# Optimization experiments

Hardware: AMD Instinct MI355X
Metric: run time of the kernel (lower is better)

## Reference

```python
import jax, jax.numpy as jnp
import numpy as np

F6_E3M2_MAX = 28.0  # max representable e3m2 value
M_TOKENS, K_IN, N_OUT = 256, 4096, 4096


def _quantize_e3m2(w: np.ndarray) -> np.ndarray:
    """Round-to-nearest onto the FP6 e3m2 grid (bias=3, min normal 2^-2, subnormal step 2^-4)."""
    sign = np.sign(w)
    a = np.minimum(np.abs(w), F6_E3M2_MAX)
    e = np.clip(np.floor(np.log2(np.maximum(a, 1e-30))), -2.0, 4.0)
    step = np.exp2(e - 2.0)  # 2 mantissa bits -> 4 steps per octave; subnormal step = 2^-4
    q = np.round(a / step) * step
    return (sign * np.minimum(q, F6_E3M2_MAX)).astype(np.float32)


def setup_inputs() -> dict:
    key = jax.random.key(0)
    k_x, k_w, k_b = jax.random.split(key, 3)
    x = (jax.random.normal(k_x, (M_TOKENS, K_IN), dtype=jnp.float32)).astype(jnp.float16)
    w_fp32 = np.asarray(jax.random.normal(k_w, (N_OUT, K_IN), dtype=jnp.float32)) * 0.02
    # per-row scale as in to_scaled_tc_float6_e3m2
    amax = np.clip(np.abs(w_fp32).max(axis=1), 1e-12, None)
    scale = F6_E3M2_MAX / amax                       # quantization scale
    weight_fp6 = _quantize_e3m2(w_fp32 * scale[:, None])  # values on the e3m2 grid
    scales = jnp.asarray(1.0 / scale, dtype=jnp.float16)  # dequant scale (stored half)
    bias = (jax.random.normal(k_b, (N_OUT,), dtype=jnp.float32) * 0.01).astype(jnp.float16)
    return {
        "x": x,
        "weight_fp6": jnp.asarray(weight_fp6),
        "scales": scales,
        "bias": bias,
    }


def reference(x, weight_fp6, scales, bias):
    # Fused dequant + GEMM: W = weight_fp6 * row_scale; out = x @ W^T + bias
    in_features = weight_fp6.shape[1]
    x2d = x.reshape(-1, in_features).astype(jnp.float16)
    w_deq = weight_fp6 * scales.astype(jnp.float32)[:, None]  # [N, K] fp32
    out = jnp.einsum("mk,nk->mn", x2d.astype(jnp.float32), w_deq,
                     preferred_element_type=jnp.float32)       # fp32 accumulate (split-K sums in fp32)
    out = out.astype(jnp.float16) + bias
    return out.reshape(*x.shape[:-1], weight_fp6.shape[0]).astype(x.dtype)
```

## Files before the change

### kernel.cpp

```cpp
#include <hip/hip_runtime.h>
#include <hip/hip_fp16.h>


typedef __attribute__((ext_vector_type(8))) _Float16 half8;
typedef __attribute__((ext_vector_type(2))) __fp16 fp16x2;
typedef __attribute__((ext_vector_type(4))) float f32x4;

typedef const __attribute__((address_space(1))) void* gptr_t;
typedef __attribute__((address_space(3))) void* lptr_t;

constexpr int K = 4096, N = 4096, M = 256;
constexpr int BM = 128, BN = 128, BK = 32;
constexpr int SPL = 8;
constexpr int KSPL = K / SPL;
constexpr int NT = KSPL / BK;

__device__ __forceinline__ void gload16(const void* g, void* l) {
    __builtin_amdgcn_global_load_lds((gptr_t)g, (lptr_t)l, 16, 0, 0);
}

__device__ __forceinline__ half8 cvt8(float4 f0, float4 f1) {
    fp16x2 p0 = __builtin_amdgcn_cvt_pkrtz(f0.x, f0.y);
    fp16x2 p1 = __builtin_amdgcn_cvt_pkrtz(f0.z, f0.w);
    fp16x2 p2 = __builtin_amdgcn_cvt_pkrtz(f1.x, f1.y);
    fp16x2 p3 = __builtin_amdgcn_cvt_pkrtz(f1.z, f1.w);
    half8 h;
    h[0]=(_Float16)p0[0]; h[1]=(_Float16)p0[1];
    h[2]=(_Float16)p1[0]; h[3]=(_Float16)p1[1];
    h[4]=(_Float16)p2[0]; h[5]=(_Float16)p2[1];
    h[6]=(_Float16)p3[0]; h[7]=(_Float16)p3[1];
    return h;
}

__global__ __launch_bounds__(256, 2)
void gemm(const float* __restrict__ X,
          const float* __restrict__ W,
          _Float16* __restrict__ P)
{
    __shared__ __align__(16) float LA[2][BM * BK];
    __shared__ __align__(16) float LB[2][BN * BK];

    const int tid = (int)threadIdx.x;
    const int l   = tid & 63;
    const int wv  = tid >> 6;
    const int lc  = l & 15;
    const int lr  = l >> 4;
    const int wm  = (wv & 1) * 64;
    const int wn  = (wv >> 1) * 64;

    const int bid = (int)blockIdx.x;
    const int xcd = bid & 7;
    const int i   = bid >> 3;
    const int mb  = i & 1;
    const int sp  = (i >> 1) & 7;
    const int nbl = i >> 4;
    const int bm  = mb * BM;
    const int bn  = (xcd * 4 + nbl) * BN;
    const int kb  = sp * KSPL;

    const int srow = wv * 32 + (l >> 3);
    const int scho = ((l & 7) ^ (l >> 3)) * 4;
    const float* ag0 = X + (size_t)(bm + srow)      * K + kb + scho;
    const float* ag1 = X + (size_t)(bm + srow + 8)  * K + kb + scho;
    const float* ag2 = X + (size_t)(bm + srow + 16) * K + kb + scho;
    const float* ag3 = X + (size_t)(bm + srow + 24) * K + kb + scho;
    const float* wg0 = W + (size_t)(bn + srow)      * K + kb + scho;
    const float* wg1 = W + (size_t)(bn + srow + 8)  * K + kb + scho;
    const float* wg2 = W + (size_t)(bn + srow + 16) * K + kb + scho;
    const float* wg3 = W + (size_t)(bn + srow + 24) * K + kb + scho;
    const int sl0 = (wv * 32 + 0)  * BK;
    const int sl1 = (wv * 32 + 8)  * BK;
    const int sl2 = (wv * 32 + 16) * BK;
    const int sl3 = (wv * 32 + 24) * BK;

#define STAGE(t, bf) do {                                               \
        gload16(ag0 + (size_t)(t) * BK, &LA[bf][sl0]);                  \
        gload16(ag1 + (size_t)(t) * BK, &LA[bf][sl1]);                  \
        gload16(ag2 + (size_t)(t) * BK, &LA[bf][sl2]);                  \
        gload16(ag3 + (size_t)(t) * BK, &LA[bf][sl3]);                  \
        gload16(wg0 + (size_t)(t) * BK, &LB[bf][sl0]);                  \
        gload16(wg1 + (size_t)(t) * BK, &LB[bf][sl1]);                  \
        gload16(wg2 + (size_t)(t) * BK, &LB[bf][sl2]);                  \
        gload16(wg3 + (size_t)(t) * BK, &LB[bf][sl3]);                  \
    } while (0)

    const int sz0 = (((lr << 1))     ^ (lc & 7)) << 2;
    const int sz1 = (((lr << 1) | 1) ^ (lc & 7)) << 2;

    f32x4 acc[4][4];
    #pragma unroll
    for (int a = 0; a < 4; ++a)
        #pragma unroll
        for (int b = 0; b < 4; ++b)
            acc[a][b] = (f32x4){0.f, 0.f, 0.f, 0.f};

#define COMPUTE(bf) do {                                                \
        half8 af[4];                                                    \
        _Pragma("unroll")                                               \
        for (int ar = 0; ar < 4; ++ar) {                                \
            const float* pa = &LA[bf][(wm + ar * 16 + lc) * BK];        \
            af[ar] = cvt8(*(const float4*)(pa + sz0),                   \
                          *(const float4*)(pa + sz1));                  \
        }                                                               \
        _Pragma("unroll")                                               \
        for (int br = 0; br < 4; ++br) {                                \
            const float* pw = &LB[bf][(wn + br * 16 + lc) * BK];        \
            half8 bb = cvt8(*(const float4*)(pw + sz0),                 \
                            *(const float4*)(pw + sz1));                \
            acc[0][br] = __builtin_amdgcn_mfma_f32_16x16x32_f16(af[0], bb, acc[0][br], 0, 0, 0); \
            acc[1][br] = __builtin_amdgcn_mfma_f32_16x16x32_f16(af[1], bb, acc[1][br], 0, 0, 0); \
            acc[2][br] = __builtin_amdgcn_mfma_f32_16x16x32_f16(af[2], bb, acc[2][br], 0, 0, 0); \
            acc[3][br] = __builtin_amdgcn_mfma_f32_16x16x32_f16(af[3], bb, acc[3][br], 0, 0, 0); \
        } } while (0)

    STAGE(0, 0);

    for (int t = 0; t < NT; ++t) {
        if (t + 1 < NT) {
            STAGE(t + 1, (t + 1) & 1);
            asm volatile("s_waitcnt vmcnt(8)" ::: "memory");
        } else {
            asm volatile("s_waitcnt vmcnt(0)" ::: "memory");
        }
        __builtin_amdgcn_sched_barrier(0);
        __builtin_amdgcn_s_barrier();
        __builtin_amdgcn_sched_barrier(0);
        COMPUTE(t & 1);
        __builtin_amdgcn_sched_barrier(0);
        __builtin_amdgcn_s_barrier();
    }
#undef STAGE
#undef COMPUTE

    _Float16* Pb = P + (size_t)sp * M * N;
    const int orow = bm + wm + lr * 4;
    const int ocol = bn + wn + lc;
    #pragma unroll
    for (int ar = 0; ar < 4; ++ar)
        #pragma unroll
        for (int br = 0; br < 4; ++br)
            #pragma unroll
            for (int r = 0; r < 4; ++r)
                Pb[(size_t)(orow + ar * 16 + r) * N + ocol + br * 16]
                    = (_Float16)acc[ar][br][r];
}

__global__ __launch_bounds__(256)
void finalize(const _Float16* __restrict__ P,
              const float* __restrict__ S,
              const float* __restrict__ Bi,
              float* __restrict__ O)
{
    const size_t i = ((size_t)blockIdx.x * 256 + threadIdx.x) * 8;
    const int n = (int)(i & (N - 1));
    float acc[8] = {0.f, 0.f, 0.f, 0.f, 0.f, 0.f, 0.f, 0.f};
    #pragma unroll
    for (int s = 0; s < SPL; ++s) {
        half8 u = *(const half8*)(P + (size_t)s * M * N + i);
        #pragma unroll
        for (int e = 0; e < 8; ++e) acc[e] += (float)u[e];
    }
    float4 sc0 = *(const float4*)(S + n);
    float4 sc1 = *(const float4*)(S + n + 4);
    float4 bb0 = *(const float4*)(Bi + n);
    float4 bb1 = *(const float4*)(Bi + n + 4);
    float sc[8] = {sc0.x, sc0.y, sc0.z, sc0.w, sc1.x, sc1.y, sc1.z, sc1.w};
    float bb[8] = {bb0.x, bb0.y, bb0.z, bb0.w, bb1.x, bb1.y, bb1.z, bb1.w};
    float out[8];
    #pragma unroll
    for (int e = 0; e < 8; ++e)
        out[e] = (float)(_Float16)((float)(_Float16)(acc[e] * sc[e]) + bb[e]);
    *(float4*)(O + i)     = (float4){out[0], out[1], out[2], out[3]};
    *(float4*)(O + i + 4) = (float4){out[4], out[5], out[6], out[7]};
}

__global__ __launch_bounds__(256)
void fp6lin_small(const float* __restrict__ X, const float* __restrict__ W,
                  const float* __restrict__ S, const float* __restrict__ Bi,
                  float* __restrict__ O)
{
    const int n = (int)blockIdx.x;
    const int m = (int)threadIdx.x;
    float s = 0.f;
    for (int k = 0; k < K; ++k)
        s += (float)(_Float16)X[(size_t)m * K + k] * (float)(_Float16)W[(size_t)n * K + k];
    O[(size_t)m * N + n] = (float)(_Float16)((float)(_Float16)(s * S[n]) + Bi[n]);
}

extern "C" void kernel_launch(void* const* d_in, const int* in_sizes, int n_in,
                              void* d_out, int out_size, void* d_ws, size_t ws_size,
                              hipStream_t stream) {
    const float* x  = (const float*)d_in[0];
    const float* w  = (const float*)d_in[1];
    const float* s  = (const float*)d_in[2];
    const float* bi = (const float*)d_in[3];
    float* o = (float*)d_out;

    const size_t pbytes = (size_t)SPL * M * N * 2;
    _Float16* P = (_Float16*)d_ws;

    if (ws_size >= pbytes) {
        gemm<<<dim3(512), dim3(256), 0, stream>>>(x, w, P);
        finalize<<<dim3(M * N / 8 / 256), dim3(256), 0, stream>>>(P, s, bi, o);
    } else {
        fp6lin_small<<<dim3(N), dim3(M), 0, stream>>>(x, w, s, bi, o);
    }
}
```

Before: 31.52 us.

## Fuse split-K reduction into GEMM via per-tile atomic counter last-block epilogue

Removes the separate finalize kernel. Each split-K block writes its partial tile, fences, and bumps a per-tile atomic counter, and the last block to arrive sums all eight partials and applies scale and bias. This saves a kernel launch and the gap between kernels, but adds a memset launch for the counters, plus atomics and a serialized reduction tail done by one block per tile.

```diff
diff --git a/kernel.cpp b/kernel.cpp
--- a/kernel.cpp
+++ b/kernel.cpp
@@ -3,6 +3,7 @@
 
 
 typedef __attribute__((ext_vector_type(8))) _Float16 half8;
+typedef __attribute__((ext_vector_type(4))) _Float16 half4;
 typedef __attribute__((ext_vector_type(2))) __fp16 fp16x2;
 typedef __attribute__((ext_vector_type(4))) float f32x4;
 
@@ -35,10 +36,15 @@
 __global__ __launch_bounds__(256, 2)
 void gemm(const float* __restrict__ X,
           const float* __restrict__ W,
-          _Float16* __restrict__ P)
+          const float* __restrict__ S,
+          const float* __restrict__ Bi,
+          float* __restrict__ O,
+          _Float16* __restrict__ P,
+          int* __restrict__ cnt)
 {
     __shared__ __align__(16) float LA[2][BM * BK];
     __shared__ __align__(16) float LB[2][BN * BK];
+    __shared__ int isWinner;
 
     const int tid = (int)threadIdx.x;
     const int l   = tid & 63;
@@ -57,6 +63,7 @@
     const int bm  = mb * BM;
     const int bn  = (xcd * 4 + nbl) * BN;
     const int kb  = sp * KSPL;
+    const int tileId = mb * 32 + (bn >> 7);
 
     const int srow = wv * 32 + (l >> 3);
     const int scho = ((l & 7) ^ (l >> 3)) * 4;
@@ -114,7 +121,6 @@
         } } while (0)
 
     STAGE(0, 0);
-
     for (int t = 0; t < NT; ++t) {
         if (t + 1 < NT) {
             STAGE(t + 1, (t + 1) & 1);
@@ -143,35 +149,38 @@
             for (int r = 0; r < 4; ++r)
                 Pb[(size_t)(orow + ar * 16 + r) * N + ocol + br * 16]
                     = (_Float16)acc[ar][br][r];
-}
-
-__global__ __launch_bounds__(256)
-void finalize(const _Float16* __restrict__ P,
-              const float* __restrict__ S,
-              const float* __restrict__ Bi,
-              float* __restrict__ O)
-{
-    const size_t i = ((size_t)blockIdx.x * 256 + threadIdx.x) * 8;
-    const int n = (int)(i & (N - 1));
-    float acc[8] = {0.f, 0.f, 0.f, 0.f, 0.f, 0.f, 0.f, 0.f};
-    #pragma unroll
-    for (int s = 0; s < SPL; ++s) {
-        half8 u = *(const half8*)(P + (size_t)s * M * N + i);
+
+    __threadfence();
+    __syncthreads();
+    if (tid == 0)
+        isWinner = (atomicAdd(&cnt[tileId], 1) == SPL - 1);
+    __syncthreads();
+    if (isWinner) {
+        __threadfence();
+        const int r0 = tid >> 5;
+        const int c0 = (tid & 31) * 4;
         #pragma unroll
-        for (int e = 0; e < 8; ++e) acc[e] += (float)u[e];
+        for (int rr = 0; rr < 16; ++rr) {
+            const int row = bm + rr * 8 + r0;
+            const int col = bn + c0;
+            float a0 = 0.f, a1 = 0.f, a2 = 0.f, a3 = 0.f;
+            #pragma unroll
+            for (int s = 0; s < SPL; ++s) {
+                half4 u = *(const half4*)(P + (size_t)s * M * N
+                                            + (size_t)row * N + col);
+                a0 += (float)u[0]; a1 += (float)u[1];
+                a2 += (float)u[2]; a3 += (float)u[3];
+            }
+            const float4 sc = *(const float4*)(S + col);
+            const float4 bb = *(const float4*)(Bi + col);
+            float4 o4;
+            o4.x = (float)(_Float16)((float)(_Float16)(a0 * sc.x) + bb.x);
+            o4.y = (float)(_Float16)((float)(_Float16)(a1 * sc.y) + bb.y);
+            o4.z = (float)(_Float16)((float)(_Float16)(a2 * sc.z) + bb.z);
+            o4.w = (float)(_Float16)((float)(_Float16)(a3 * sc.w) + bb.w);
+            *(float4*)(O + (size_t)row * N + col) = o4;
+        }
     }
-    float4 sc0 = *(const float4*)(S + n);
-    float4 sc1 = *(const float4*)(S + n + 4);
-    float4 bb0 = *(const float4*)(Bi + n);
-    float4 bb1 = *(const float4*)(Bi + n + 4);
-    float sc[8] = {sc0.x, sc0.y, sc0.z, sc0.w, sc1.x, sc1.y, sc1.z, sc1.w};
-    float bb[8] = {bb0.x, bb0.y, bb0.z, bb0.w, bb1.x, bb1.y, bb1.z, bb1.w};
-    float out[8];
-    #pragma unroll
-    for (int e = 0; e < 8; ++e)
-        out[e] = (float)(_Float16)((float)(_Float16)(acc[e] * sc[e]) + bb[e]);
-    *(float4*)(O + i)     = (float4){out[0], out[1], out[2], out[3]};
-    *(float4*)(O + i + 4) = (float4){out[4], out[5], out[6], out[7]};
 }
 
 __global__ __launch_bounds__(256)
@@ -197,11 +206,12 @@
     float* o = (float*)d_out;
 
     const size_t pbytes = (size_t)SPL * M * N * 2;
-    _Float16* P = (_Float16*)d_ws;
-
-    if (ws_size >= pbytes) {
-        gemm<<<dim3(512), dim3(256), 0, stream>>>(x, w, P);
-        finalize<<<dim3(M * N / 8 / 256), dim3(256), 0, stream>>>(P, s, bi, o);
+    _Float16* P  = (_Float16*)d_ws;
+    int* cnt     = (int*)((char*)d_ws + pbytes);
+
+    if (ws_size >= pbytes + 64 * sizeof(int)) {
+        hipMemsetAsync(cnt, 0, 64 * sizeof(int), stream);
+        gemm<<<dim3(512), dim3(256), 0, stream>>>(x, w, s, bi, o, P, cnt);
     } else {
         fp6lin_small<<<dim3(N), dim3(M), 0, stream>>>(x, w, s, bi, o);
     }
```

After: 121.6 us. 3.86x slower.

## Switch GEMM to barrier-free single-wave 64x64 tiles with 4-way split-K

Applied to the files above, without the earlier changes.

The 256-thread, 128x128-tile GEMM becomes 1024 blocks of a single 64-thread wave, each computing a 64x64 tile. Split-K drops from 8 to 4, which halves the fp16 partial buffer written by the GEMM and read back by the finalize kernel. With only one wave per block, the LDS s_barriers are removed and only a waitcnt synchronises the double buffer. In exchange, each tile reuses loaded data less, so W is re-read by four M-blocks instead of two. There are also few waves per CU to hide memory latency.

```diff
diff --git a/kernel.cpp b/kernel.cpp
--- a/kernel.cpp
+++ b/kernel.cpp
@@ -10,8 +10,8 @@
 typedef __attribute__((address_space(3))) void* lptr_t;
 
 constexpr int K = 4096, N = 4096, M = 256;
-constexpr int BM = 128, BN = 128, BK = 32;
-constexpr int SPL = 8;
+constexpr int BK = 32;
+constexpr int SPL = 4;
 constexpr int KSPL = K / SPL;
 constexpr int NT = KSPL / BK;
 
@@ -32,57 +32,41 @@
     return h;
 }
 
-__global__ __launch_bounds__(256, 2)
+__global__ __launch_bounds__(64, 1)
 void gemm(const float* __restrict__ X,
           const float* __restrict__ W,
           _Float16* __restrict__ P)
 {
-    __shared__ __align__(16) float LA[2][BM * BK];
-    __shared__ __align__(16) float LB[2][BN * BK];
+    __shared__ __align__(16) float LA[2][64 * BK];
+    __shared__ __align__(16) float LB[2][64 * BK];
 
-    const int tid = (int)threadIdx.x;
-    const int l   = tid & 63;
-    const int wv  = tid >> 6;
-    const int lc  = l & 15;
-    const int lr  = l >> 4;
-    const int wm  = (wv & 1) * 64;
-    const int wn  = (wv >> 1) * 64;
+    const int l  = (int)threadIdx.x;
+    const int lc = l & 15;
+    const int lr = l >> 4;
 
     const int bid = (int)blockIdx.x;
     const int xcd = bid & 7;
     const int i   = bid >> 3;
-    const int mb  = i & 1;
-    const int sp  = (i >> 1) & 7;
+    const int mb  = i & 3;
+    const int sp  = (i >> 2) & 3;
     const int nbl = i >> 4;
-    const int bm  = mb * BM;
-    const int bn  = (xcd * 4 + nbl) * BN;
+    const int bm  = mb * 64;
+    const int bn  = (xcd * 8 + nbl) * 64;
     const int kb  = sp * KSPL;
 
-    const int srow = wv * 32 + (l >> 3);
-    const int scho = ((l & 7) ^ (l >> 3)) * 4;
-    const float* ag0 = X + (size_t)(bm + srow)      * K + kb + scho;
-    const float* ag1 = X + (size_t)(bm + srow + 8)  * K + kb + scho;
-    const float* ag2 = X + (size_t)(bm + srow + 16) * K + kb + scho;
-    const float* ag3 = X + (size_t)(bm + srow + 24) * K + kb + scho;
-    const float* wg0 = W + (size_t)(bn + srow)      * K + kb + scho;
-    const float* wg1 = W + (size_t)(bn + srow + 8)  * K + kb + scho;
-    const float* wg2 = W + (size_t)(bn + srow + 16) * K + kb + scho;
-    const float* wg3 = W + (size_t)(bn + srow + 24) * K + kb + scho;
-    const int sl0 = (wv * 32 + 0)  * BK;
-    const int sl1 = (wv * 32 + 8)  * BK;
-    const int sl2 = (wv * 32 + 16) * BK;
-    const int sl3 = (wv * 32 + 24) * BK;
+    const int srow = l >> 3;
+    const int sch  = ((l & 7) ^ (l >> 3)) * 4;
+    const float* ax = X + (size_t)(bm + srow) * K + kb + sch;
+    const float* wx = W + (size_t)(bn + srow) * K + kb + sch;
 
-#define STAGE(t, bf) do {                                               \
-        gload16(ag0 + (size_t)(t) * BK, &LA[bf][sl0]);                  \
-        gload16(ag1 + (size_t)(t) * BK, &LA[bf][sl1]);                  \
-        gload16(ag2 + (size_t)(t) * BK, &LA[bf][sl2]);                  \
-        gload16(ag3 + (size_t)(t) * BK, &LA[bf][sl3]);                  \
-        gload16(wg0 + (size_t)(t) * BK, &LB[bf][sl0]);                  \
-        gload16(wg1 + (size_t)(t) * BK, &LB[bf][sl1]);                  \
-        gload16(wg2 + (size_t)(t) * BK, &LB[bf][sl2]);                  \
-        gload16(wg3 + (size_t)(t) * BK, &LB[bf][sl3]);                  \
-    } while (0)
+#define STAGE(t, bf) do {                                                \
+        _Pragma("unroll")                                                \
+        for (int s = 0; s < 8; ++s) {                                    \
+            gload16(ax + (size_t)(s * 8) * K + (size_t)(t) * BK,         \
+                    &LA[bf][s * 256]);                                   \
+            gload16(wx + (size_t)(s * 8) * K + (size_t)(t) * BK,         \
+                    &LB[bf][s * 256]);                                   \
+        } } while (0)
 
     const int sz0 = (((lr << 1))     ^ (lc & 7)) << 2;
     const int sz1 = (((lr << 1) | 1) ^ (lc & 7)) << 2;
@@ -94,19 +78,19 @@
         for (int b = 0; b < 4; ++b)
             acc[a][b] = (f32x4){0.f, 0.f, 0.f, 0.f};
 
-#define COMPUTE(bf) do {                                                \
-        half8 af[4];                                                    \
-        _Pragma("unroll")                                               \
-        for (int ar = 0; ar < 4; ++ar) {                                \
-            const float* pa = &LA[bf][(wm + ar * 16 + lc) * BK];        \
-            af[ar] = cvt8(*(const float4*)(pa + sz0),                   \
-                          *(const float4*)(pa + sz1));                  \
-        }                                                               \
-        _Pragma("unroll")                                               \
-        for (int br = 0; br < 4; ++br) {                                \
-            const float* pw = &LB[bf][(wn + br * 16 + lc) * BK];        \
-            half8 bb = cvt8(*(const float4*)(pw + sz0),                 \
-                            *(const float4*)(pw + sz1));                \
+#define COMPUTE(bf) do {                                                 \
+        half8 af[4];                                                     \
+        _Pragma("unroll")                                                \
+        for (int ar = 0; ar < 4; ++ar) {                                 \
+            const float* pa = &LA[bf][(ar * 16 + lc) * BK];              \
+            af[ar] = cvt8(*(const float4*)(pa + sz0),                    \
+                          *(const float4*)(pa + sz1));                   \
+        }                                                                \
+        _Pragma("unroll")                                                \
+        for (int br = 0; br < 4; ++br) {                                 \
+            const float* pw = &LB[bf][(br * 16 + lc) * BK];              \
+            half8 bb = cvt8(*(const float4*)(pw + sz0),                  \
+                            *(const float4*)(pw + sz1));                 \
             acc[0][br] = __builtin_amdgcn_mfma_f32_16x16x32_f16(af[0], bb, acc[0][br], 0, 0, 0); \
             acc[1][br] = __builtin_amdgcn_mfma_f32_16x16x32_f16(af[1], bb, acc[1][br], 0, 0, 0); \
             acc[2][br] = __builtin_amdgcn_mfma_f32_16x16x32_f16(af[2], bb, acc[2][br], 0, 0, 0); \
@@ -114,27 +98,24 @@
         } } while (0)
 
     STAGE(0, 0);
-
     for (int t = 0; t < NT; ++t) {
         if (t + 1 < NT) {
             STAGE(t + 1, (t + 1) & 1);
-            asm volatile("s_waitcnt vmcnt(8)" ::: "memory");
+            __builtin_amdgcn_sched_barrier(0);
+            asm volatile("s_waitcnt vmcnt(16)" ::: "memory");
         } else {
             asm volatile("s_waitcnt vmcnt(0)" ::: "memory");
         }
         __builtin_amdgcn_sched_barrier(0);
-        __builtin_amdgcn_s_barrier();
-        __builtin_amdgcn_sched_barrier(0);
         COMPUTE(t & 1);
         __builtin_amdgcn_sched_barrier(0);
-        __builtin_amdgcn_s_barrier();
     }
 #undef STAGE
 #undef COMPUTE
 
     _Float16* Pb = P + (size_t)sp * M * N;
-    const int orow = bm + wm + lr * 4;
-    const int ocol = bn + wn + lc;
+    const int orow = bm + lr * 4;
+    const int ocol = bn + lc;
     #pragma unroll
     for (int ar = 0; ar < 4; ++ar)
         #pragma unroll
@@ -200,7 +181,7 @@
     _Float16* P = (_Float16*)d_ws;
 
     if (ws_size >= pbytes) {
-        gemm<<<dim3(512), dim3(256), 0, stream>>>(x, w, P);
+        gemm<<<dim3(1024), dim3(64), 0, stream>>>(x, w, P);
         finalize<<<dim3(M * N / 8 / 256), dim3(256), 0, stream>>>(P, s, bi, o);
     } else {
         fp6lin_small<<<dim3(N), dim3(M), 0, stream>>>(x, w, s, bi, o);
```

Measured after the change: 40.83 us. +29.5%, slower.

## Convert fp32 tiles to fp16 in registers before LDS store, prefetching two tiles ahead

Applied to the files above, without the earlier changes.

Replaces the direct global-to-LDS fp32 loads with register loads that are converted to fp16 once and then stored to LDS. MFMA operands are then read straight from LDS as half8, with no per-use conversion. Before, each wave re-converted the fp32 tile it read, so the same elements were converted several times and twice as many LDS bytes were moved. Two register stages give a prefetch depth of two tiles, at the cost of higher VGPR pressure. The XOR swizzle is dropped, which may bring LDS bank conflicts.

```diff
diff --git a/kernel.cpp b/kernel.cpp
--- a/kernel.cpp
+++ b/kernel.cpp
@@ -3,11 +3,9 @@
 
 
 typedef __attribute__((ext_vector_type(8))) _Float16 half8;
+typedef __attribute__((ext_vector_type(4))) _Float16 half4;
 typedef __attribute__((ext_vector_type(2))) __fp16 fp16x2;
 typedef __attribute__((ext_vector_type(4))) float f32x4;
-
-typedef const __attribute__((address_space(1))) void* gptr_t;
-typedef __attribute__((address_space(3))) void* lptr_t;
 
 constexpr int K = 4096, N = 4096, M = 256;
 constexpr int BM = 128, BN = 128, BK = 32;
@@ -15,20 +13,12 @@
 constexpr int KSPL = K / SPL;
 constexpr int NT = KSPL / BK;
 
-__device__ __forceinline__ void gload16(const void* g, void* l) {
-    __builtin_amdgcn_global_load_lds((gptr_t)g, (lptr_t)l, 16, 0, 0);
-}
-
-__device__ __forceinline__ half8 cvt8(float4 f0, float4 f1) {
-    fp16x2 p0 = __builtin_amdgcn_cvt_pkrtz(f0.x, f0.y);
-    fp16x2 p1 = __builtin_amdgcn_cvt_pkrtz(f0.z, f0.w);
-    fp16x2 p2 = __builtin_amdgcn_cvt_pkrtz(f1.x, f1.y);
-    fp16x2 p3 = __builtin_amdgcn_cvt_pkrtz(f1.z, f1.w);
-    half8 h;
+__device__ __forceinline__ half4 cvt4(float4 f) {
+    fp16x2 p0 = __builtin_amdgcn_cvt_pkrtz(f.x, f.y);
+    fp16x2 p1 = __builtin_amdgcn_cvt_pkrtz(f.z, f.w);
+    half4 h;
     h[0]=(_Float16)p0[0]; h[1]=(_Float16)p0[1];
     h[2]=(_Float16)p1[0]; h[3]=(_Float16)p1[1];
-    h[4]=(_Float16)p2[0]; h[5]=(_Float16)p2[1];
-    h[6]=(_Float16)p3[0]; h[7]=(_Float16)p3[1];
     return h;
 }
 
@@ -37,8 +27,8 @@
           const float* __restrict__ W,
           _Float16* __restrict__ P)
 {
-    __shared__ __align__(16) float LA[2][BM * BK];
-    __shared__ __align__(16) float LB[2][BN * BK];
+    __shared__ __align__(16) _Float16 LA[2][BM * BK];
+    __shared__ __align__(16) _Float16 LB[2][BN * BK];
 
     const int tid = (int)threadIdx.x;
     const int l   = tid & 63;
@@ -59,33 +49,48 @@
     const int kb  = sp * KSPL;
 
     const int srow = wv * 32 + (l >> 3);
-    const int scho = ((l & 7) ^ (l >> 3)) * 4;
-    const float* ag0 = X + (size_t)(bm + srow)      * K + kb + scho;
-    const float* ag1 = X + (size_t)(bm + srow + 8)  * K + kb + scho;
-    const float* ag2 = X + (size_t)(bm + srow + 16) * K + kb + scho;
-    const float* ag3 = X + (size_t)(bm + srow + 24) * K + kb + scho;
-    const float* wg0 = W + (size_t)(bn + srow)      * K + kb + scho;
-    const float* wg1 = W + (size_t)(bn + srow + 8)  * K + kb + scho;
-    const float* wg2 = W + (size_t)(bn + srow + 16) * K + kb + scho;
-    const float* wg3 = W + (size_t)(bn + srow + 24) * K + kb + scho;
-    const int sl0 = (wv * 32 + 0)  * BK;
-    const int sl1 = (wv * 32 + 8)  * BK;
-    const int sl2 = (wv * 32 + 16) * BK;
-    const int sl3 = (wv * 32 + 24) * BK;
-
-#define STAGE(t, bf) do {                                               \
-        gload16(ag0 + (size_t)(t) * BK, &LA[bf][sl0]);                  \
-        gload16(ag1 + (size_t)(t) * BK, &LA[bf][sl1]);                  \
-        gload16(ag2 + (size_t)(t) * BK, &LA[bf][sl2]);                  \
-        gload16(ag3 + (size_t)(t) * BK, &LA[bf][sl3]);                  \
-        gload16(wg0 + (size_t)(t) * BK, &LB[bf][sl0]);                  \
-        gload16(wg1 + (size_t)(t) * BK, &LB[bf][sl1]);                  \
-        gload16(wg2 + (size_t)(t) * BK, &LB[bf][sl2]);                  \
-        gload16(wg3 + (size_t)(t) * BK, &LB[bf][sl3]);                  \
-    } while (0)
-
-    const int sz0 = (((lr << 1))     ^ (lc & 7)) << 2;
-    const int sz1 = (((lr << 1) | 1) ^ (lc & 7)) << 2;
+    const int scol = (l & 7) * 4;
+    const float* ax0 = X + (size_t)(bm + srow)      * K + kb + scol;
+    const float* ax1 = X + (size_t)(bm + srow + 8)  * K + kb + scol;
+    const float* ax2 = X + (size_t)(bm + srow + 16) * K + kb + scol;
+    const float* ax3 = X + (size_t)(bm + srow + 24) * K + kb + scol;
+    const float* wx0 = W + (size_t)(bn + srow)      * K + kb + scol;
+    const float* wx1 = W + (size_t)(bn + srow + 8)  * K + kb + scol;
+    const float* wx2 = W + (size_t)(bn + srow + 16) * K + kb + scol;
+    const float* wx3 = W + (size_t)(bn + srow + 24) * K + kb + scol;
+    const int wr0 = srow * BK + (l & 7) * 4;
+
+    float4 s0a0, s0a1, s0a2, s0a3, s0w0, s0w1, s0w2, s0w3;
+    float4 s1a0, s1a1, s1a2, s1a3, s1w0, s1w1, s1w2, s1w3;
+
+#define GLOAD0(t) do { const size_t o = (size_t)(t) * BK;               \
+        s0a0 = *(const float4*)(ax0 + o); s0a1 = *(const float4*)(ax1 + o); \
+        s0a2 = *(const float4*)(ax2 + o); s0a3 = *(const float4*)(ax3 + o); \
+        s0w0 = *(const float4*)(wx0 + o); s0w1 = *(const float4*)(wx1 + o); \
+        s0w2 = *(const float4*)(wx2 + o); s0w3 = *(const float4*)(wx3 + o); } while (0)
+#define GLOAD1(t) do { const size_t o = (size_t)(t) * BK;               \
+        s1a0 = *(const float4*)(ax0 + o); s1a1 = *(const float4*)(ax1 + o); \
+        s1a2 = *(const float4*)(ax2 + o); s1a3 = *(const float4*)(ax3 + o); \
+        s1w0 = *(const float4*)(wx0 + o); s1w1 = *(const float4*)(wx1 + o); \
+        s1w2 = *(const float4*)(wx2 + o); s1w3 = *(const float4*)(wx3 + o); } while (0)
+#define CVTW0(bf) do {                                                  \
+        *(half4*)(&LA[bf][wr0])          = cvt4(s0a0);                  \
+        *(half4*)(&LA[bf][wr0 + 8*BK])   = cvt4(s0a1);                  \
+        *(half4*)(&LA[bf][wr0 + 16*BK])  = cvt4(s0a2);                  \
+        *(half4*)(&LA[bf][wr0 + 24*BK])  = cvt4(s0a3);                  \
+        *(half4*)(&LB[bf][wr0])          = cvt4(s0w0);                  \
+        *(half4*)(&LB[bf][wr0 + 8*BK])   = cvt4(s0w1);                  \
+        *(half4*)(&LB[bf][wr0 + 16*BK])  = cvt4(s0w2);                  \
+        *(half4*)(&LB[bf][wr0 + 24*BK])  = cvt4(s0w3); } while (0)
+#define CVTW1(bf) do {                                                  \
+        *(half4*)(&LA[bf][wr0])          = cvt4(s1a0);                  \
+        *(half4*)(&LA[bf][wr0 + 8*BK])   = cvt4(s1a1);                  \
+        *(half4*)(&LA[bf][wr0 + 16*BK])  = cvt4(s1a2);                  \
+        *(half4*)(&LA[bf][wr0 + 24*BK])  = cvt4(s1a3);                  \
+        *(half4*)(&LB[bf][wr0])          = cvt4(s1w0);                  \
+        *(half4*)(&LB[bf][wr0 + 8*BK])   = cvt4(s1w1);                  \
+        *(half4*)(&LB[bf][wr0 + 16*BK])  = cvt4(s1w2);                  \
+        *(half4*)(&LB[bf][wr0 + 24*BK])  = cvt4(s1w3); } while (0)
 
     f32x4 acc[4][4];
     #pragma unroll
@@ -95,41 +100,42 @@
             acc[a][b] = (f32x4){0.f, 0.f, 0.f, 0.f};
 
 #define COMPUTE(bf) do {                                                \
-        half8 af[4];                                                    \
+        half8 af[4], wf[4];                                             \
         _Pragma("unroll")                                               \
-        for (int ar = 0; ar < 4; ++ar) {                                \
-            const float* pa = &LA[bf][(wm + ar * 16 + lc) * BK];        \
-            af[ar] = cvt8(*(const float4*)(pa + sz0),                   \
-                          *(const float4*)(pa + sz1));                  \
-        }                                                               \
+        for (int ar = 0; ar < 4; ++ar)                                  \
+            af[ar] = *(const half8*)(&LA[bf][(wm + ar * 16 + lc) * BK + lr * 8]); \
         _Pragma("unroll")                                               \
-        for (int br = 0; br < 4; ++br) {                                \
-            const float* pw = &LB[bf][(wn + br * 16 + lc) * BK];        \
-            half8 bb = cvt8(*(const float4*)(pw + sz0),                 \
-                            *(const float4*)(pw + sz1));                \
-            acc[0][br] = __builtin_amdgcn_mfma_f32_16x16x32_f16(af[0], bb, acc[0][br], 0, 0, 0); \
-            acc[1][br] = __builtin_amdgcn_mfma_f32_16x16x32_f16(af[1], bb, acc[1][br], 0, 0, 0); \
-            acc[2][br] = __builtin_amdgcn_mfma_f32_16x16x32_f16(af[2], bb, acc[2][br], 0, 0, 0); \
-            acc[3][br] = __builtin_amdgcn_mfma_f32_16x16x32_f16(af[3], bb, acc[3][br], 0, 0, 0); \
-        } } while (0)
-
-    STAGE(0, 0);
+        for (int br = 0; br < 4; ++br)                                  \
+            wf[br] = *(const half8*)(&LB[bf][(wn + br * 16 + lc) * BK + lr * 8]); \
+        _Pragma("unroll")                                               \
+        for (int ar = 0; ar < 4; ++ar)                                  \
+            _Pragma("unroll")                                           \
+            for (int br = 0; br < 4; ++br)                              \
+                acc[ar][br] = __builtin_amdgcn_mfma_f32_16x16x32_f16(   \
+                    af[ar], wf[br], acc[ar][br], 0, 0, 0); } while (0)
+
+    GLOAD0(0);
+    GLOAD1(1);
+    asm volatile("s_waitcnt vmcnt(8)" ::: "memory");
+    CVTW0(0);
+    asm volatile("s_waitcnt lgkmcnt(0)" ::: "memory");
+    __builtin_amdgcn_s_barrier();
 
     for (int t = 0; t < NT; ++t) {
-        if (t + 1 < NT) {
-            STAGE(t + 1, (t + 1) & 1);
-            asm volatile("s_waitcnt vmcnt(8)" ::: "memory");
-        } else {
-            asm volatile("s_waitcnt vmcnt(0)" ::: "memory");
-        }
-        __builtin_amdgcn_sched_barrier(0);
-        __builtin_amdgcn_s_barrier();
+        const int tn = (t + 2 < NT) ? t + 2 : NT - 1;
+        if (t & 1) GLOAD1(tn); else GLOAD0(tn);
         __builtin_amdgcn_sched_barrier(0);
         COMPUTE(t & 1);
+        asm volatile("s_waitcnt vmcnt(8)" ::: "memory");
         __builtin_amdgcn_sched_barrier(0);
+        if (t & 1) CVTW0((t + 1) & 1); else CVTW1((t + 1) & 1);
+        asm volatile("s_waitcnt lgkmcnt(0)" ::: "memory");
         __builtin_amdgcn_s_barrier();
     }
-#undef STAGE
+#undef GLOAD0
+#undef GLOAD1
+#undef CVTW0
+#undef CVTW1
 #undef COMPUTE
 
     _Float16* Pb = P + (size_t)sp * M * N;
```

New measurement: 33.17 us. +5.2%, slower.
